# Kernel tuning notes

Measured on AMD Instinct MI355X. Metric: run time of the kernel, lower is better.

Reference implementation:

```python
import jax, jax.numpy as jnp
import numpy as np

N = 1048576
D = 128
NUM_GRAPHS = 4096

def setup_inputs() -> dict:
    key = jax.random.key(0)
    k1, k2 = jax.random.split(key)
    x = jax.random.normal(k1, (N, D), dtype=jnp.float32)
    batch = jnp.sort(jax.random.randint(k2, (N,), 0, NUM_GRAPHS, dtype=jnp.int64))
    return {"x": x, "batch": batch, "num_graphs": NUM_GRAPHS}

def reference(x, batch, num_graphs):
    # Single-pass scatter-mean: segment_sum of features and of counts.
    seg_sum = jax.ops.segment_sum(x, batch, num_segments=num_graphs)          # (B, D)
    counts = jax.ops.segment_sum(jnp.ones((x.shape[0],), x.dtype), batch,
                                 num_segments=num_graphs)                      # (B,)
    # Avoid div-by-zero for (rare) empty segments; torch would yield NaN there.
    safe = jnp.maximum(counts, 1.0)
    return seg_sum / safe[:, None]
```

## Files before the change

kernel.cpp:

```cpp
#include <hip/hip_runtime.h>
#include <hip/hip_bf16.h>


#define D       128
#define D4      32
#define RPB     512
#define THREADS 256
#define RIF     8
#define UNROLL  4

typedef float v4f __attribute__((ext_vector_type(4)));

__device__ __forceinline__ void flush_acc(float* __restrict__ out,
                                          int seg, int col, const v4f& acc) {
    float* o = out + (size_t)seg * D + col * 4;
    atomicAdd(o + 0, acc.x);
    atomicAdd(o + 1, acc.y);
    atomicAdd(o + 2, acc.z);
    atomicAdd(o + 3, acc.w);
}

__device__ __forceinline__ void step_row(const int* __restrict__ sbatch, int i,
                                         v4f v, int col,
                                         float* __restrict__ out,
                                         int& cur, v4f& acc) {
    int seg = sbatch[i];
    if (seg != cur) {
        if (cur >= 0) flush_acc(out, cur, col, acc);
        cur = seg;
        acc = (v4f){0.f, 0.f, 0.f, 0.f};
    }
    acc += v;
}

__global__ __launch_bounds__(THREADS)
void pool_sum_kernel(const v4f* __restrict__ x,
                     const int* __restrict__ batch,
                     float* __restrict__ out,
                     int n_rows) {
    __shared__ int sbatch[RPB];
    const int base = blockIdx.x * RPB;
    const int tid  = threadIdx.x;

    for (int i = tid; i < RPB; i += THREADS) {
        int r = base + i;
        sbatch[i] = (r < n_rows) ? batch[r] : -1;
    }
    __syncthreads();

    const int col = tid & (D4 - 1);
    const int rl  = tid >> 5;

    v4f acc = (v4f){0.f, 0.f, 0.f, 0.f};
    int cur = -1;

    const int nloc = n_rows - base;

    if (nloc >= RPB) {
        const v4f* p = x + (size_t)(base + rl) * D4 + col;
        for (int i = rl; i < RPB; i += UNROLL * RIF) {
            v4f v0 = __builtin_nontemporal_load(p + 0 * RIF * D4);
            v4f v1 = __builtin_nontemporal_load(p + 1 * RIF * D4);
            v4f v2 = __builtin_nontemporal_load(p + 2 * RIF * D4);
            v4f v3 = __builtin_nontemporal_load(p + 3 * RIF * D4);
            step_row(sbatch, i + 0 * RIF, v0, col, out, cur, acc);
            step_row(sbatch, i + 1 * RIF, v1, col, out, cur, acc);
            step_row(sbatch, i + 2 * RIF, v2, col, out, cur, acc);
            step_row(sbatch, i + 3 * RIF, v3, col, out, cur, acc);
            p += UNROLL * RIF * D4;
        }
    } else {
        for (int i = rl; i < nloc; i += RIF) {
            v4f v = __builtin_nontemporal_load(x + (size_t)(base + i) * D4 + col);
            step_row(sbatch, i, v, col, out, cur, acc);
        }
    }
    if (cur >= 0) flush_acc(out, cur, col, acc);
}

__device__ __forceinline__ int lower_bound_dev(const int* __restrict__ a,
                                               int n, int v) {
    int lo = 0, hi = n;
    while (lo < hi) {
        int mid = (lo + hi) >> 1;
        if (a[mid] < v) lo = mid + 1; else hi = mid;
    }
    return lo;
}

__global__ __launch_bounds__(D)
void pool_div_kernel(float* __restrict__ out,
                     const int* __restrict__ batch,
                     int n_rows) {
    const int s = blockIdx.x;
    __shared__ float cnt_s;
    if (threadIdx.x == 0) {
        int lo = lower_bound_dev(batch, n_rows, s);
        int hi = lower_bound_dev(batch, n_rows, s + 1);
        int cnt = hi - lo;
        cnt_s = (float)(cnt > 1 ? cnt : 1);
    }
    __syncthreads();
    size_t idx = (size_t)s * D + threadIdx.x;
    out[idx] = out[idx] / cnt_s;
}

extern "C" void kernel_launch(void* const* d_in, const int* in_sizes, int n_in,
                              void* d_out, int out_size, void* d_ws, size_t ws_size,
                              hipStream_t stream) {
    const v4f* x      = (const v4f*)d_in[0];
    const int* batch  = (const int*)d_in[1];
    float* out        = (float*)d_out;

    const int n_rows     = in_sizes[0] / D;
    const int num_graphs = out_size / D;

    hipMemsetAsync(d_out, 0, (size_t)out_size * sizeof(float), stream);

    int blocks = (n_rows + RPB - 1) / RPB;
    pool_sum_kernel<<<blocks, THREADS, 0, stream>>>(x, batch, out, n_rows);
    pool_div_kernel<<<num_graphs, D, 0, stream>>>(out, batch, n_rows);
}
```

Measured before the change: 712.3 us.

## Fuse scatter-mean into one segment-per-block kernel using binary-searched bounds

Replaces the memset, the atomic row-block sum kernel and the separate divide kernel with a single kernel. Each block binary-searches its segment's row range in the sorted batch array, reduces those rows across 8 row lanes, combines the lanes in shared memory, scales by the inverse count and writes the result directly. This removes the float atomics, the output zeroing and two launches. Load balance now depends on segment sizes, which relies on batch being sorted.

```diff
diff --git a/kernel.cpp b/kernel.cpp
--- a/kernel.cpp
+++ b/kernel.cpp
@@ -4,83 +4,14 @@
 
 #define D       128
 #define D4      32
-#define RPB     512
 #define THREADS 256
 #define RIF     8
 #define UNROLL  4
 
 typedef float v4f __attribute__((ext_vector_type(4)));
 
-__device__ __forceinline__ void flush_acc(float* __restrict__ out,
-                                          int seg, int col, const v4f& acc) {
-    float* o = out + (size_t)seg * D + col * 4;
-    atomicAdd(o + 0, acc.x);
-    atomicAdd(o + 1, acc.y);
-    atomicAdd(o + 2, acc.z);
-    atomicAdd(o + 3, acc.w);
-}
-
-__device__ __forceinline__ void step_row(const int* __restrict__ sbatch, int i,
-                                         v4f v, int col,
-                                         float* __restrict__ out,
-                                         int& cur, v4f& acc) {
-    int seg = sbatch[i];
-    if (seg != cur) {
-        if (cur >= 0) flush_acc(out, cur, col, acc);
-        cur = seg;
-        acc = (v4f){0.f, 0.f, 0.f, 0.f};
-    }
-    acc += v;
-}
-
-__global__ __launch_bounds__(THREADS)
-void pool_sum_kernel(const v4f* __restrict__ x,
-                     const int* __restrict__ batch,
-                     float* __restrict__ out,
-                     int n_rows) {
-    __shared__ int sbatch[RPB];
-    const int base = blockIdx.x * RPB;
-    const int tid  = threadIdx.x;
-
-    for (int i = tid; i < RPB; i += THREADS) {
-        int r = base + i;
-        sbatch[i] = (r < n_rows) ? batch[r] : -1;
-    }
-    __syncthreads();
-
-    const int col = tid & (D4 - 1);
-    const int rl  = tid >> 5;
-
-    v4f acc = (v4f){0.f, 0.f, 0.f, 0.f};
-    int cur = -1;
-
-    const int nloc = n_rows - base;
-
-    if (nloc >= RPB) {
-        const v4f* p = x + (size_t)(base + rl) * D4 + col;
-        for (int i = rl; i < RPB; i += UNROLL * RIF) {
-            v4f v0 = __builtin_nontemporal_load(p + 0 * RIF * D4);
-            v4f v1 = __builtin_nontemporal_load(p + 1 * RIF * D4);
-            v4f v2 = __builtin_nontemporal_load(p + 2 * RIF * D4);
-            v4f v3 = __builtin_nontemporal_load(p + 3 * RIF * D4);
-            step_row(sbatch, i + 0 * RIF, v0, col, out, cur, acc);
-            step_row(sbatch, i + 1 * RIF, v1, col, out, cur, acc);
-            step_row(sbatch, i + 2 * RIF, v2, col, out, cur, acc);
-            step_row(sbatch, i + 3 * RIF, v3, col, out, cur, acc);
-            p += UNROLL * RIF * D4;
-        }
-    } else {
-        for (int i = rl; i < nloc; i += RIF) {
-            v4f v = __builtin_nontemporal_load(x + (size_t)(base + i) * D4 + col);
-            step_row(sbatch, i, v, col, out, cur, acc);
-        }
-    }
-    if (cur >= 0) flush_acc(out, cur, col, acc);
-}
-
 __device__ __forceinline__ int lower_bound_dev(const int* __restrict__ a,
-                                               int n, int v) {
-    int lo = 0, hi = n;
+                                               int lo, int hi, int v) {
     while (lo < hi) {
         int mid = (lo + hi) >> 1;
         if (a[mid] < v) lo = mid + 1; else hi = mid;
@@ -88,21 +19,50 @@
     return lo;
 }
 
-__global__ __launch_bounds__(D)
-void pool_div_kernel(float* __restrict__ out,
-                     const int* __restrict__ batch,
-                     int n_rows) {
+__global__ __launch_bounds__(THREADS)
+void pool_mean_kernel(const v4f* __restrict__ x,
+                      const int* __restrict__ batch,
+                      float* __restrict__ out,
+                      int n_rows) {
     const int s = blockIdx.x;
-    __shared__ float cnt_s;
-    if (threadIdx.x == 0) {
-        int lo = lower_bound_dev(batch, n_rows, s);
-        int hi = lower_bound_dev(batch, n_rows, s + 1);
-        int cnt = hi - lo;
-        cnt_s = (float)(cnt > 1 ? cnt : 1);
+
+    const int lo = lower_bound_dev(batch, 0, n_rows, s);
+    const int hi = lower_bound_dev(batch, lo, n_rows, s + 1);
+    const int cnt = hi - lo;
+    const float inv = 1.0f / (float)(cnt > 1 ? cnt : 1);
+
+    const int col = threadIdx.x & (D4 - 1);
+    const int rl  = threadIdx.x >> 5;
+
+    v4f acc = (v4f){0.f, 0.f, 0.f, 0.f};
+
+    int i = lo + rl;
+    const v4f* p = x + (size_t)i * D4 + col;
+    for (; i + (UNROLL - 1) * RIF < hi; i += UNROLL * RIF) {
+        v4f v0 = __builtin_nontemporal_load(p + 0 * RIF * D4);
+        v4f v1 = __builtin_nontemporal_load(p + 1 * RIF * D4);
+        v4f v2 = __builtin_nontemporal_load(p + 2 * RIF * D4);
+        v4f v3 = __builtin_nontemporal_load(p + 3 * RIF * D4);
+        acc += v0; acc += v1; acc += v2; acc += v3;
+        p += UNROLL * RIF * D4;
     }
+    for (; i < hi; i += RIF) {
+        acc += __builtin_nontemporal_load(p);
+        p += RIF * D4;
+    }
+
+    __shared__ v4f partials[RIF][D4];
+    partials[rl][col] = acc;
     __syncthreads();
-    size_t idx = (size_t)s * D + threadIdx.x;
-    out[idx] = out[idx] / cnt_s;
+
+    if (threadIdx.x < D4) {
+        v4f t = partials[0][col];
+        #pragma unroll
+        for (int r = 1; r < RIF; ++r) t += partials[r][col];
+        t *= inv;
+        v4f* o = (v4f*)out + (size_t)s * D4 + col;
+        __builtin_nontemporal_store(t, o);
+    }
 }
 
 extern "C" void kernel_launch(void* const* d_in, const int* in_sizes, int n_in,
@@ -115,9 +75,5 @@
     const int n_rows     = in_sizes[0] / D;
     const int num_graphs = out_size / D;
 
-    hipMemsetAsync(d_out, 0, (size_t)out_size * sizeof(float), stream);
-
-    int blocks = (n_rows + RPB - 1) / RPB;
-    pool_sum_kernel<<<blocks, THREADS, 0, stream>>>(x, batch, out, n_rows);
-    pool_div_kernel<<<num_graphs, D, 0, stream>>>(out, batch, n_rows);
+    pool_mean_kernel<<<num_graphs, THREADS, 0, stream>>>(x, batch, out, n_rows);
 }
```

Result: faster. 656.5 us (-7.8%).
